# Optimization experiments

Measured on AMD Instinct MI355X. Metric: run time of the kernel, lower is better.

## Reference

```python
import jax, jax.numpy as jnp
import numpy as np

N_NODES = 75000
N_EDGES = 1200000
DIM = 64


def setup_inputs() -> dict:
    key = jax.random.key(0)
    ks = jax.random.split(key, 9)
    d_u = jax.random.normal(ks[0], (N_NODES, DIM), dtype=jnp.float32)
    p_u = jax.random.normal(ks[1], (N_NODES, DIM), dtype=jnp.float32)
    s = 1.0 / np.sqrt(DIM)
    w_q = jax.random.normal(ks[2], (DIM, DIM), dtype=jnp.float32) * s
    w_k = jax.random.normal(ks[3], (DIM, DIM), dtype=jnp.float32) * s
    w_v = jax.random.normal(ks[4], (DIM, DIM), dtype=jnp.float32) * s
    e1 = jax.random.normal(ks[5], (DIM,), dtype=jnp.float32) * s
    e2 = jax.random.normal(ks[6], (DIM,), dtype=jnp.float32) * s
    src = jax.random.randint(ks[7], (N_EDGES,), 0, N_NODES, dtype=jnp.int32)
    dst = jax.random.randint(ks[8], (N_EDGES,), 0, N_NODES, dtype=jnp.int32)
    return {"d_u": d_u, "p_u": p_u, "w_q": w_q, "w_k": w_k, "w_v": w_v,
            "e1": e1, "e2": e2, "src": src, "dst": dst}


def reference(d_u, p_u, w_q, w_k, w_v, e1, e2, src, dst):
    n_nodes = d_u.shape[0]
    # per-node edge scores: e1(w_k(p_u)) on src side, e2(w_q(d_u)) on dst side
    h_src = (p_u @ w_k.T) @ e1            # [N]
    h_dst = (d_u @ w_q.T) @ e2            # [N]
    # apply_edges(u_add_v): c_e = h_src[u] + h_dst[v], shape [E]
    c = h_src[src] + h_dst[dst]
    # EdgeWeightNorm(norm='right'): divide by sum of incoming edge weights at dst
    denom = jax.ops.segment_sum(c, dst, num_segments=n_nodes)  # [N]
    c = c / denom[dst]
    # update_all(u_mul_e, sum): messages w_v(p_u)[u] * c_e, summed at dst
    wv = p_u @ w_v.T                      # [N, D]
    msg = wv[src] * c[:, None]            # [E, D]
    out = jax.ops.segment_sum(msg, dst, num_segments=n_nodes)  # [N, D]
    return out
```

## Files before the change

kernel.cpp:

```cpp
#include <hip/hip_runtime.h>

#define N_NODES 75000
#define N_EDGES 1200000
#define DIM 64
#define SCAN_BLK 1024
#define N_SCAN_BLKS ((N_NODES + SCAN_BLK - 1) / SCAN_BLK)
#define NCOPY 8
#define HIST_BLOCKS ((N_EDGES + 1023) / 1024)
#define PRE_GROUPS ((HIST_BLOCKS + 7) / 8)
#define WAVE_SLOTS (PRE_GROUPS * 8)
#define PRE_BLKS (PRE_GROUPS * 16)

__device__ __forceinline__ float lane_bcf(float v, int l) {
    return __int_as_float(__builtin_amdgcn_readlane(__float_as_int(v), l));
}
__device__ __forceinline__ int lane_bci(int v, int l) {
    return __builtin_amdgcn_readlane(v, l);
}

__global__ void vec_precompute(const float* __restrict__ w_q,
                               const float* __restrict__ w_k,
                               const float* __restrict__ e1,
                               const float* __restrict__ e2,
                               double* __restrict__ a,
                               double* __restrict__ b) {
    int t = threadIdx.x;
    if (t < DIM) {
        double s = 0.0;
        #pragma unroll
        for (int j = 0; j < DIM; ++j) s += (double)e1[j] * (double)w_k[j * DIM + t];
        a[t] = s;
    } else if (t < 2 * DIM) {
        int d = t - DIM;
        double s = 0.0;
        #pragma unroll
        for (int j = 0; j < DIM; ++j) s += (double)e2[j] * (double)w_q[j * DIM + d];
        b[d] = s;
    }
}

__global__ __launch_bounds__(256, 4) void fused_pre(
    const int* __restrict__ dst, int* __restrict__ cnt8,
    int* __restrict__ rank,
    const float* __restrict__ d_u, const float* __restrict__ p_u,
    const float* __restrict__ w_v,
    const double* __restrict__ a_vec, const double* __restrict__ b_vec,
    double* __restrict__ h_src, double* __restrict__ h_dst,
    float* __restrict__ wv_out) {
    int g = blockIdx.x >> 4;
    int slot = blockIdx.x & 15;
    if (slot < 8) {
        int hb = g * 8 + slot;
        if (hb >= HIST_BLOCKS) return;
        int base = hb << 10;
        int* mycnt = cnt8 + (size_t)(hb & (NCOPY - 1)) * N_NODES;
        #pragma unroll
        for (int k = 0; k < 4; ++k) {
            int e = base + k * 256 + threadIdx.x;
            if (e < N_EDGES) rank[e] = atomicAdd(&mycnt[dst[e]], 1);
        }
    } else {
        int wb = g * 8 + (slot - 8);
        int lane = threadIdx.x & 63;
        int wave = wb * 4 + (threadIdx.x >> 6);
        const int nwaves = WAVE_SLOTS * 4;

        float w[DIM];
        const float4* wr = (const float4*)(w_v + (size_t)lane * DIM);
        #pragma unroll
        for (int k = 0; k < DIM / 4; ++k) {
            float4 v = wr[k];
            w[4 * k + 0] = v.x; w[4 * k + 1] = v.y;
            w[4 * k + 2] = v.z; w[4 * k + 3] = v.w;
        }
        double al = a_vec[lane];
        double bl = b_vec[lane];

        for (int i = wave; i < N_NODES; i += nwaves) {
            float pl = p_u[(size_t)i * DIM + lane];
            float dl = d_u[(size_t)i * DIM + lane];

            double hs = (double)pl * al;
            #pragma unroll
            for (int off = 32; off > 0; off >>= 1) hs += __shfl_xor(hs, off, 64);
            double hd = (double)dl * bl;
            #pragma unroll
            for (int off = 32; off > 0; off >>= 1) hd += __shfl_xor(hd, off, 64);
            if (lane == 0) { h_src[i] = hs; h_dst[i] = hd; }

            float a0 = 0.f, a1 = 0.f, a2 = 0.f, a3 = 0.f;
            #pragma unroll
            for (int d = 0; d < DIM; d += 4) {
                a0 += w[d + 0] * lane_bcf(pl, d + 0);
                a1 += w[d + 1] * lane_bcf(pl, d + 1);
                a2 += w[d + 2] * lane_bcf(pl, d + 2);
                a3 += w[d + 3] * lane_bcf(pl, d + 3);
            }
            wv_out[(size_t)i * DIM + lane] = (a0 + a1) + (a2 + a3);
        }
    }
}

__global__ __launch_bounds__(SCAN_BLK) void scan1_kernel(
    int* __restrict__ cnt8, int* __restrict__ cnt,
    int* __restrict__ row, int* __restrict__ bsum) {
    __shared__ int sh[SCAN_BLK];
    int tid = threadIdx.x;
    int i = blockIdx.x * SCAN_BLK + tid;
    int v = 0;
    if (i < N_NODES) {
        int run = 0;
        #pragma unroll
        for (int c = 0; c < NCOPY; ++c) {
            int x = cnt8[(size_t)c * N_NODES + i];
            cnt8[(size_t)c * N_NODES + i] = run;
            run += x;
        }
        v = run;
        cnt[i] = run;
    }
    sh[tid] = v;
    __syncthreads();
    for (int off = 1; off < SCAN_BLK; off <<= 1) {
        int t = (tid >= off) ? sh[tid - off] : 0;
        __syncthreads();
        sh[tid] += t;
        __syncthreads();
    }
    if (i < N_NODES) row[i] = sh[tid] - v;
    if (tid == SCAN_BLK - 1) bsum[blockIdx.x] = sh[tid];
}

__global__ __launch_bounds__(256) void scan23_kernel(
    int* __restrict__ row, const int* __restrict__ bsum) {
    __shared__ int pref[N_SCAN_BLKS];
    int tid = threadIdx.x;
    if (tid == 0) {
        int run = 0;
        #pragma unroll 8
        for (int k = 0; k < N_SCAN_BLKS; ++k) { pref[k] = run; run += bsum[k]; }
    }
    __syncthreads();
    int i = blockIdx.x * 256 + tid;
    if (i >= N_NODES) return;
    row[i] += pref[i / SCAN_BLK];
}

__global__ __launch_bounds__(256) void build_kernel(
    const int* __restrict__ src, const int* __restrict__ dst,
    const int* __restrict__ row, const int* __restrict__ cnt8,
    const int* __restrict__ rank, int* __restrict__ csr_src) {
    int e = blockIdx.x * 256 + threadIdx.x;
    if (e >= N_EDGES) return;
    int d = dst[e];
    int copy = (e >> 10) & (NCOPY - 1);
    int pos = row[d] + cnt8[(size_t)copy * N_NODES + d] + rank[e];
    csr_src[pos] = src[e];
}

__global__ __launch_bounds__(256) void node_gather(
    const int* __restrict__ row, const int* __restrict__ cnt,
    const int* __restrict__ csr_src,
    const double* __restrict__ h_src, const double* __restrict__ h_dst,
    const float* __restrict__ wv, float* __restrict__ out) {
    int gtid = blockIdx.x * 256 + threadIdx.x;
    int node = gtid >> 6;
    int lane = threadIdx.x & 63;
    if (node >= N_NODES) return;

    int start = row[node];
    int deg = cnt[node];
    double hd = h_dst[node];

    if (deg <= 64) {
        int s0 = 0;
        double c0 = 0.0;
        if (lane < deg) {
            s0 = csr_src[start + lane];
            c0 = h_src[s0] + hd;
        }
        double r = c0;
        #pragma unroll
        for (int off = 32; off > 0; off >>= 1) r += __shfl_xor(r, off, 64);
        double inv = 1.0 / r;
        float cf0 = (lane < deg) ? (float)(c0 * inv) : 0.f;

        float acc = 0.f;
        int j = 0;
        for (; j + 8 <= deg; j += 8) {
            int   s[8];
            float c[8];
            #pragma unroll
            for (int k = 0; k < 8; ++k) {
                s[k] = lane_bci(s0, j + k);
                c[k] = lane_bcf(cf0, j + k);
            }
            float wl[8];
            #pragma unroll
            for (int k = 0; k < 8; ++k)
                wl[k] = wv[(size_t)s[k] * DIM + lane];
            #pragma unroll
            for (int k = 0; k < 8; ++k)
                acc += wl[k] * c[k];
        }
        for (; j < deg; ++j) {
            int s = lane_bci(s0, j); float cf = lane_bcf(cf0, j);
            acc += wv[(size_t)s * DIM + lane] * cf;
        }
        out[(size_t)node * DIM + lane] = acc;
    } else {
        double denom = 0.0;
        for (int base = 0; base < deg; base += 64) {
            int m = deg - base; if (m > 64) m = 64;
            double c = 0.0;
            if (lane < m) {
                int s = csr_src[start + base + lane];
                c = h_src[s] + hd;
            }
            #pragma unroll
            for (int off = 32; off > 0; off >>= 1) c += __shfl_xor(c, off, 64);
            denom += c;
        }
        double inv = 1.0 / denom;
        float acc = 0.f;
        for (int base = 0; base < deg; base += 64) {
            int m = deg - base; if (m > 64) m = 64;
            int s1 = 0; float cf1 = 0.f;
            if (lane < m) {
                s1 = csr_src[start + base + lane];
                cf1 = (float)((h_src[s1] + hd) * inv);
            }
            for (int j = 0; j < m; ++j) {
                int s = lane_bci(s1, j);
                float cf = lane_bcf(cf1, j);
                acc += wv[(size_t)s * DIM + lane] * cf;
            }
        }
        out[(size_t)node * DIM + lane] = acc;
    }
}

extern "C" void kernel_launch(void* const* d_in, const int* in_sizes, int n_in,
                              void* d_out, int out_size, void* d_ws, size_t ws_size,
                              hipStream_t stream) {
    const float* d_u = (const float*)d_in[0];
    const float* p_u = (const float*)d_in[1];
    const float* w_q = (const float*)d_in[2];
    const float* w_k = (const float*)d_in[3];
    const float* w_v = (const float*)d_in[4];
    const float* e1  = (const float*)d_in[5];
    const float* e2  = (const float*)d_in[6];
    const int*   src = (const int*)d_in[7];
    const int*   dst = (const int*)d_in[8];
    float* out = (float*)d_out;

    double* a      = (double*)d_ws;
    double* b      = a + DIM;
    double* h_src  = b + DIM;
    double* h_dst  = h_src + N_NODES;
    float*  wv     = (float*)(h_dst + N_NODES);
    int*    cnt    = (int*)(wv + (size_t)N_NODES * DIM);
    int*    row    = cnt + N_NODES;
    int*    bsum   = row + N_NODES;
    int*    cnt8   = bsum + 128;
    int*    rank   = cnt8 + (size_t)NCOPY * N_NODES;
    int*    csr_src= rank + N_EDGES;

    hipMemsetAsync(cnt8, 0, sizeof(int) * (size_t)NCOPY * N_NODES, stream);

    vec_precompute<<<1, 128, 0, stream>>>(w_q, w_k, e1, e2, a, b);

    fused_pre<<<PRE_BLKS, 256, 0, stream>>>(
        dst, cnt8, rank, d_u, p_u, w_v, a, b, h_src, h_dst, wv);

    scan1_kernel<<<N_SCAN_BLKS, SCAN_BLK, 0, stream>>>(cnt8, cnt, row, bsum);
    scan23_kernel<<<(N_NODES + 255) / 256, 256, 0, stream>>>(row, bsum);

    build_kernel<<<(N_EDGES + 255) / 256, 256, 0, stream>>>(
        src, dst, row, cnt8, rank, csr_src);

    node_gather<<<(N_NODES * 64 + 255) / 256, 256, 0, stream>>>(
        row, cnt, csr_src, h_src, h_dst, wv, out);
}
```

Before: 263.1 us.

## Fold memset into init kernel and fuse scan fixup into consumers

Replaces the hipMemsetAsync plus single-block vector precompute with one init kernel that zeroes the per-copy histograms and computes the projection vectors. Removes the separate scan fixup kernel; build and gather kernels each recompute the block-sum prefix in shared memory and add it when reading row offsets. This cuts two launches and one pass over row, at the cost of a serial 74-element prefix loop in thread 0 of every block of build and gather, which stalls each block before its main work.

```diff
diff --git a/kernel.cpp b/kernel.cpp
--- a/kernel.cpp
+++ b/kernel.cpp
@@ -10,6 +10,7 @@
 #define PRE_GROUPS ((HIST_BLOCKS + 7) / 8)
 #define WAVE_SLOTS (PRE_GROUPS * 8)
 #define PRE_BLKS (PRE_GROUPS * 16)
+#define INIT_BLKS 1172
 
 __device__ __forceinline__ float lane_bcf(float v, int l) {
     return __int_as_float(__builtin_amdgcn_readlane(__float_as_int(v), l));
@@ -18,24 +19,30 @@
     return __builtin_amdgcn_readlane(v, l);
 }
 
-__global__ void vec_precompute(const float* __restrict__ w_q,
-                               const float* __restrict__ w_k,
-                               const float* __restrict__ e1,
-                               const float* __restrict__ e2,
-                               double* __restrict__ a,
-                               double* __restrict__ b) {
-    int t = threadIdx.x;
-    if (t < DIM) {
-        double s = 0.0;
-        #pragma unroll
-        for (int j = 0; j < DIM; ++j) s += (double)e1[j] * (double)w_k[j * DIM + t];
-        a[t] = s;
-    } else if (t < 2 * DIM) {
-        int d = t - DIM;
-        double s = 0.0;
-        #pragma unroll
-        for (int j = 0; j < DIM; ++j) s += (double)e2[j] * (double)w_q[j * DIM + d];
-        b[d] = s;
+__global__ __launch_bounds__(256) void init_kernel(
+    const float* __restrict__ w_q, const float* __restrict__ w_k,
+    const float* __restrict__ e1, const float* __restrict__ e2,
+    double* __restrict__ a, double* __restrict__ b,
+    int* __restrict__ cnt8) {
+    int gtid = blockIdx.x * 256 + threadIdx.x;
+    const int NT = INIT_BLKS * 256;
+    for (int i = gtid; i < NCOPY * N_NODES; i += NT) cnt8[i] = 0;
+    if (blockIdx.x == 0) {
+        int t = threadIdx.x;
+        if (t < DIM) {
+            double s = 0.0;
+            #pragma unroll
+            for (int j = 0; j < DIM; ++j)
+                s += (double)e1[j] * (double)w_k[j * DIM + t];
+            a[t] = s;
+        } else if (t < 2 * DIM) {
+            int d = t - DIM;
+            double s = 0.0;
+            #pragma unroll
+            for (int j = 0; j < DIM; ++j)
+                s += (double)e2[j] * (double)w_q[j * DIM + d];
+            b[d] = s;
+        }
     }
 }
 
@@ -131,44 +138,46 @@
     if (tid == SCAN_BLK - 1) bsum[blockIdx.x] = sh[tid];
 }
 
-__global__ __launch_bounds__(256) void scan23_kernel(
-    int* __restrict__ row, const int* __restrict__ bsum) {
+__global__ __launch_bounds__(256) void build_kernel(
+    const int* __restrict__ src, const int* __restrict__ dst,
+    const int* __restrict__ row, const int* __restrict__ bsum,
+    const int* __restrict__ cnt8,
+    const int* __restrict__ rank, int* __restrict__ csr_src) {
     __shared__ int pref[N_SCAN_BLKS];
-    int tid = threadIdx.x;
-    if (tid == 0) {
+    if (threadIdx.x == 0) {
         int run = 0;
         #pragma unroll 8
         for (int k = 0; k < N_SCAN_BLKS; ++k) { pref[k] = run; run += bsum[k]; }
     }
     __syncthreads();
-    int i = blockIdx.x * 256 + tid;
-    if (i >= N_NODES) return;
-    row[i] += pref[i / SCAN_BLK];
-}
-
-__global__ __launch_bounds__(256) void build_kernel(
-    const int* __restrict__ src, const int* __restrict__ dst,
-    const int* __restrict__ row, const int* __restrict__ cnt8,
-    const int* __restrict__ rank, int* __restrict__ csr_src) {
     int e = blockIdx.x * 256 + threadIdx.x;
     if (e >= N_EDGES) return;
     int d = dst[e];
     int copy = (e >> 10) & (NCOPY - 1);
-    int pos = row[d] + cnt8[(size_t)copy * N_NODES + d] + rank[e];
+    int pos = row[d] + pref[d >> 10] + cnt8[(size_t)copy * N_NODES + d] + rank[e];
     csr_src[pos] = src[e];
 }
 
 __global__ __launch_bounds__(256) void node_gather(
     const int* __restrict__ row, const int* __restrict__ cnt,
+    const int* __restrict__ bsum,
     const int* __restrict__ csr_src,
     const double* __restrict__ h_src, const double* __restrict__ h_dst,
     const float* __restrict__ wv, float* __restrict__ out) {
+    __shared__ int pref[N_SCAN_BLKS];
+    if (threadIdx.x == 0) {
+        int run = 0;
+        #pragma unroll 8
+        for (int k = 0; k < N_SCAN_BLKS; ++k) { pref[k] = run; run += bsum[k]; }
+    }
+    __syncthreads();
+
     int gtid = blockIdx.x * 256 + threadIdx.x;
     int node = gtid >> 6;
     int lane = threadIdx.x & 63;
     if (node >= N_NODES) return;
 
-    int start = row[node];
+    int start = row[node] + pref[node >> 10];
     int deg = cnt[node];
     double hd = h_dst[node];
 
@@ -266,19 +275,16 @@
     int*    rank   = cnt8 + (size_t)NCOPY * N_NODES;
     int*    csr_src= rank + N_EDGES;
 
-    hipMemsetAsync(cnt8, 0, sizeof(int) * (size_t)NCOPY * N_NODES, stream);
-
-    vec_precompute<<<1, 128, 0, stream>>>(w_q, w_k, e1, e2, a, b);
+    init_kernel<<<INIT_BLKS, 256, 0, stream>>>(w_q, w_k, e1, e2, a, b, cnt8);
 
     fused_pre<<<PRE_BLKS, 256, 0, stream>>>(
         dst, cnt8, rank, d_u, p_u, w_v, a, b, h_src, h_dst, wv);
 
     scan1_kernel<<<N_SCAN_BLKS, SCAN_BLK, 0, stream>>>(cnt8, cnt, row, bsum);
-    scan23_kernel<<<(N_NODES + 255) / 256, 256, 0, stream>>>(row, bsum);
 
     build_kernel<<<(N_EDGES + 255) / 256, 256, 0, stream>>>(
-        src, dst, row, cnt8, rank, csr_src);
+        src, dst, row, bsum, cnt8, rank, csr_src);
 
     node_gather<<<(N_NODES * 64 + 255) / 256, 256, 0, stream>>>(
-        row, cnt, csr_src, h_src, h_dst, wv, out);
-}
+        row, cnt, bsum, csr_src, h_src, h_dst, wv, out);
+}
```

After: 267.5 us. Within noise of the previous version (+1.7%).
